# Optimization experiments

Hardware: AMD Instinct MI355X
Metric: run time of the kernel (lower is better)

The kernel has to match this reference:

```python
import jax, jax.numpy as jnp
import numpy as np

B, S, D, H, NK = 2, 512, 256, 8, 16
DK = D // H
NEG = -1e32


def _layer_norm(x, g, b, eps=1e-5):
    m = jnp.mean(x, axis=-1, keepdims=True)
    v = jnp.var(x, axis=-1, keepdims=True)
    return (x - m) / jnp.sqrt(v + eps) * g + b


def _attention(q, k, v, mask, gamma, maxout):
    # q,k,v: [b,h,s,dk]; mask: [1,1,s,s] bool; gamma: [h,1,1]
    d_k = q.shape[-1]
    scores = jnp.einsum('bhqd,bhkd->bhqk', q, k) / float(np.sqrt(d_k))
    s = scores.shape[-1]
    # gamma exp-decay branch (at=None in practice -> position_effect path)
    sm = jax.nn.softmax(jnp.where(mask, scores, NEG), axis=-1)
    distcum = jnp.cumsum(sm, axis=-1)
    disttotal = jnp.sum(sm, axis=-1, keepdims=True)
    idx = jnp.arange(s, dtype=scores.dtype)
    pos = jnp.abs(idx[None, :] - idx[:, None])[None, None]  # |x1 - x2|
    dist = jax.lax.stop_gradient(
        jnp.sqrt(jnp.clip((disttotal - distcum) * pos, 0.0, None)))
    g = -jnp.abs(gamma)[None]  # [1,h,1,1]
    total_effect = jnp.clip(jnp.exp(dist * g), 1e-5, 1e5)
    scores = scores * total_effect
    scores = jax.nn.softmax(jnp.where(mask, scores, NEG), axis=-1)
    scores = jnp.where(mask, scores, 0.0)
    if maxout:
        scale = jnp.minimum(1.0 / jnp.max(scores, axis=-1, keepdims=True), 5.0)
        scores = scores * scale
    out = jnp.einsum('bhqk,bhkd->bhqd', scores, v)
    return out, scores


def _mha(qx, kx, vx, mask, Wq, bq, Wk, bk, Wv, bv, Wo, bo, gammas, maxout):
    b, s, d = qx.shape
    def proj(x, W, bb):
        return (x @ W.T + bb).reshape(b, s, H, DK).transpose(0, 2, 1, 3)
    q = proj(qx, Wq, bq)
    k = proj(kx, Wk, bk)
    v = proj(vx, Wv, bv)
    out, scores = _attention(q, k, v, mask, gammas, maxout)
    concat = out.transpose(0, 2, 1, 3).reshape(b, s, d)
    return concat @ Wo.T + bo, scores


def _layer(qx, kx, vx, mask, Wq, bq, Wk, bk, Wv, bv, Wo, bo, gammas, ln_g, ln_b, maxout):
    out, scores = _mha(qx, kx, vx, mask, Wq, bq, Wk, bk, Wv, bv, Wo, bo, gammas, maxout)
    return _layer_norm(qx + out, ln_g, ln_b), scores  # dropout=identity in eval


def setup_inputs() -> dict:
    key = jax.random.key(0)
    ks = iter(jax.random.split(key, 40))
    def W(shp, sc=0.05):
        return jax.random.normal(next(ks), shp, jnp.float32) * sc
    return dict(
        q_emb=jax.random.normal(next(ks), (B, S, D), jnp.float32),
        s_emb=jax.random.normal(next(ks), (B, S, D), jnp.float32),
        s_emb_extr=jax.random.normal(next(ks), (B, S, D), jnp.float32),
        lens=jax.random.randint(next(ks), (B,), 1, S),
        at=jax.random.randint(next(ks), (B, S), 0, 300),
        Wq1=W((D, D)), bq1=jnp.zeros((D,)), Wv1=W((D, D)), bv1=jnp.zeros((D,)),
        Wo1=W((D, D)), bo1=jnp.zeros((D,)), gam1=W((H, 1, 1), 0.3),
        ln1_g=jnp.ones((D,)), ln1_b=jnp.zeros((D,)),
        Wq4=W((D, D)), bq4=jnp.zeros((D,)), Wk4=W((D, D)), bk4=jnp.zeros((D,)),
        Wv4=W((D, D)), bv4=jnp.zeros((D,)),
        Wo4=W((D, D)), bo4=jnp.zeros((D,)), gam4=W((H, 1, 1), 0.3),
        ln4_g=jnp.ones((D,)), ln4_b=jnp.zeros((D,)),
        know_params=jax.random.uniform(next(ks), (NK, D), jnp.float32, -1.0, 1.0),
    )


def reference(q_emb, s_emb, s_emb_extr, lens, at,
              Wq1, bq1, Wv1, bv1, Wo1, bo1, gam1, ln1_g, ln1_b,
              Wq4, bq4, Wk4, bk4, Wv4, bv4, Wo4, bo4, gam4, ln4_g, ln4_b,
              know_params):
    bs, s, d = q_emb.shape
    tri = jnp.tril(jnp.ones((s, s), bool), 0)[None, None]       # peek_cur=True
    tri_strict = jnp.tril(jnp.ones((s, s), bool), -1)[None, None]  # peek_cur=False
    # block1: kq_same -> k_linear is q_linear; maxout=False
    p, q_scores = _layer(q_emb, q_emb, s_emb, tri,
                         Wq1, bq1, Wq1, bq1, Wv1, bv1, Wo1, bo1, gam1,
                         ln1_g, ln1_b, maxout=False)
    # expand knowledge queries: [bs*NK, s, d]
    query = jnp.broadcast_to(know_params[None, :, None, :], (bs, NK, s, d)).reshape(bs * NK, s, d)
    hq = jnp.broadcast_to(q_emb[:, None], (bs, NK, s, d)).reshape(bs * NK, s, d)
    pe = jnp.broadcast_to(p[:, None], (bs, NK, s, d)).reshape(bs * NK, s, d)
    # block4: kq_same=False; maxout=True
    z, k_scores = _layer(query, hq, pe, tri_strict,
                         Wq4, bq4, Wk4, bk4, Wv4, bv4, Wo4, bo4, gam4,
                         ln4_g, ln4_b, maxout=True)
    z = z.reshape(bs, NK, s, d).transpose(0, 2, 1, 3).reshape(bs, s, NK * d)
    k_scores = k_scores.reshape(bs, NK, H, s, s).transpose(0, 2, 3, 1, 4)
    return z, q_scores, k_scores
```

## Files before the change

### kernel.cpp

```cpp
#include <hip/hip_runtime.h>


namespace {
constexpr int kB = 2, kS = 512, kD = 256, kH = 8, kDK = 32, kNK = 16;
constexpr float kScale = 0.17677669529663687f;
constexpr int kPS = 520;
}

typedef unsigned short u16;
typedef u16 u16x4 __attribute__((ext_vector_type(4)));
typedef u16 u16x8 __attribute__((ext_vector_type(8)));
typedef short s16x8 __attribute__((ext_vector_type(8)));
typedef float f32x4 __attribute__((ext_vector_type(4)));

__device__ __forceinline__ float bf2f(u16 u) { return __uint_as_float(((unsigned)u) << 16); }
__device__ __forceinline__ u16 f2bf(float f) {
    unsigned u = __float_as_uint(f);
    return (u16)((u + 0x7fffu + ((u >> 16) & 1u)) >> 16);
}

__device__ __forceinline__ float wave_max64(float v) {
#pragma unroll
    for (int off = 32; off; off >>= 1) v = fmaxf(v, __shfl_xor(v, off));
    return v;
}
__device__ __forceinline__ float wave_sum64(float v) {
#pragma unroll
    for (int off = 32; off; off >>= 1) v += __shfl_xor(v, off);
    return v;
}

__global__ __launch_bounds__(256) void wt_kernel(const float* __restrict__ W0,
                                                 const float* __restrict__ W1,
                                                 const float* __restrict__ W2,
                                                 const float* __restrict__ W3,
                                                 const float* __restrict__ W4,
                                                 const float* __restrict__ W5,
                                                 float* __restrict__ WT) {
    const float* srcs[6] = {W0, W1, W2, W3, W4, W5};
    const float* W = srcs[blockIdx.y];
    float* T = WT + (size_t)blockIdx.y * kD * kD;
    const int k = blockIdx.x, c = threadIdx.x;
    T[(size_t)k * kD + c] = W[(size_t)c * kD + k];
}

__global__ __launch_bounds__(256) void vt4_kernel(const float* __restrict__ V4,
                                                  u16* __restrict__ Vtg) {
    __shared__ float tile[128][33];
    const int bh = blockIdx.x, kt = blockIdx.y;
    const int t = threadIdx.x;
    const float* src = V4 + ((size_t)bh * kS + kt * 128) * kDK;
    for (int i = t * 4; i < 128 * 32; i += 1024) {
        f32x4 v = *(const f32x4*)(src + i);
        const int k = i >> 5, d = i & 31;
        tile[k][d] = v[0]; tile[k][d + 1] = v[1];
        tile[k][d + 2] = v[2]; tile[k][d + 3] = v[3];
    }
    __syncthreads();
    const int d = t >> 3, kc = (t & 7) * 16;
    u16* dst = Vtg + ((size_t)bh * kDK + d) * kS + kt * 128 + kc;
    u16x8 o1, o2;
#pragma unroll
    for (int j = 0; j < 8; ++j) o1[j] = f2bf(tile[kc + j][d]);
#pragma unroll
    for (int j = 0; j < 8; ++j) o2[j] = f2bf(tile[kc + 8 + j][d]);
    *(u16x8*)dst = o1;
    *(u16x8*)(dst + 8) = o2;
}

template <int RPW, int MODE>
__global__ __launch_bounds__(256) void gemm256(const float* __restrict__ X,
                                               const float* __restrict__ WT,
                                               const float* __restrict__ bias,
                                               const float* __restrict__ extra,
                                               const float* __restrict__ lng,
                                               const float* __restrict__ lnb,
                                               float* __restrict__ Y) {
    constexpr int TM = RPW * 4;
    __shared__ float xs[TM][kD];
    const int t = threadIdx.x;
    const int r0 = blockIdx.x * TM;

    if (MODE == 0) {
#pragma unroll
        for (int it = 0; it < RPW; ++it) {
            const int idx = it * 1024 + t * 4;
            const int r = idx >> 8, c = idx & 255;
            *(f32x4*)&xs[r][c] = *(const f32x4*)(X + (size_t)(r0 + r) * kD + c);
        }
    } else {
#pragma unroll
        for (int it = 0; it < RPW; ++it) {
            const int chunk = it * 32 + (t >> 3);
            const int r = chunk >> 3, h = chunk & 7;
            const int row = r0 + r;
            const float* src = X + (((size_t)(row >> 9) * kH + h) * kS + (row & (kS - 1))) * kDK + (t & 7) * 4;
            *(f32x4*)&xs[r][h * kDK + (t & 7) * 4] = *(const f32x4*)src;
        }
    }
    __syncthreads();

    const int wv = t >> 6;
    const int c4 = (t & 63) * 4;
    float acc[RPW][4];
    {
        f32x4 bv = *(const f32x4*)(bias + c4);
#pragma unroll
        for (int r = 0; r < RPW; ++r)
#pragma unroll
            for (int j = 0; j < 4; ++j) acc[r][j] = bv[j];
    }
    for (int k0 = 0; k0 < kD; k0 += 4) {
        f32x4 w0 = *(const f32x4*)(WT + (size_t)(k0 + 0) * kD + c4);
        f32x4 w1 = *(const f32x4*)(WT + (size_t)(k0 + 1) * kD + c4);
        f32x4 w2 = *(const f32x4*)(WT + (size_t)(k0 + 2) * kD + c4);
        f32x4 w3 = *(const f32x4*)(WT + (size_t)(k0 + 3) * kD + c4);
#pragma unroll
        for (int r = 0; r < RPW; ++r) {
            f32x4 xv = *(const f32x4*)&xs[wv * RPW + r][k0];
#pragma unroll
            for (int cc = 0; cc < 4; ++cc) {
                acc[r][cc] = fmaf(xv[0], w0[cc], acc[r][cc]);
                acc[r][cc] = fmaf(xv[1], w1[cc], acc[r][cc]);
                acc[r][cc] = fmaf(xv[2], w2[cc], acc[r][cc]);
                acc[r][cc] = fmaf(xv[3], w3[cc], acc[r][cc]);
            }
        }
    }

#pragma unroll
    for (int r = 0; r < RPW; ++r) {
        const int row = r0 + wv * RPW + r;
        if (MODE == 0) {
            const int h = c4 >> 5, dk = c4 & 31;
            *(f32x4*)(Y + (((size_t)(row >> 9) * kH + h) * kS + (row & (kS - 1))) * kDK + dk) =
                *(f32x4*)acc[r];
        } else {
            f32x4 x;
            if (MODE == 1) {
                f32x4 e = *(const f32x4*)(extra + (size_t)row * kD + c4);
#pragma unroll
                for (int j = 0; j < 4; ++j) x[j] = acc[r][j] + e[j];
            } else {
                const int nk = (row >> 9) & (kNK - 1);
                f32x4 e = *(const f32x4*)(extra + (size_t)nk * kD + c4);
#pragma unroll
                for (int j = 0; j < 4; ++j) x[j] = acc[r][j] + e[j];
            }
            float s1 = x[0] + x[1] + x[2] + x[3];
            float s2 = x[0] * x[0] + x[1] * x[1] + x[2] * x[2] + x[3] * x[3];
#pragma unroll
            for (int off = 32; off; off >>= 1) {
                s1 += __shfl_xor(s1, off);
                s2 += __shfl_xor(s2, off);
            }
            const float mean = s1 * (1.f / kD);
            const float var = s2 * (1.f / kD) - mean * mean;
            const float rstd = rsqrtf(var + 1e-5f);
            f32x4 g = *(const f32x4*)(lng + c4);
            f32x4 bb = *(const f32x4*)(lnb + c4);
            f32x4 y;
#pragma unroll
            for (int j = 0; j < 4; ++j) y[j] = (x[j] - mean) * rstd * g[j] + bb[j];
            if (MODE == 1) {
                *(f32x4*)(Y + (size_t)row * kD + c4) = y;
            } else {
                const int bnk = row >> 9, s = row & (kS - 1);
                const int nk = bnk & (kNK - 1), b = bnk >> 4;
                *(f32x4*)(Y + (((size_t)(b * kS + s) * kNK + nk) * kD) + c4) = y;
            }
        }
    }
}

__global__ __launch_bounds__(256) void gemm256_b3(const float* __restrict__ X0,
                                                  const float* __restrict__ WT0,
                                                  const float* __restrict__ b0,
                                                  float* __restrict__ Y0,
                                                  const float* __restrict__ X1,
                                                  const float* __restrict__ WT1,
                                                  const float* __restrict__ b1,
                                                  float* __restrict__ Y1,
                                                  const float* __restrict__ X2,
                                                  const float* __restrict__ WT2,
                                                  const float* __restrict__ b2,
                                                  float* __restrict__ Y2) {
    __shared__ float xs[4][kD];
    const float* X = (blockIdx.y == 0) ? X0 : (blockIdx.y == 1) ? X1 : X2;
    const float* WT = (blockIdx.y == 0) ? WT0 : (blockIdx.y == 1) ? WT1 : WT2;
    const float* bias = (blockIdx.y == 0) ? b0 : (blockIdx.y == 1) ? b1 : b2;
    float* Y = (blockIdx.y == 0) ? Y0 : (blockIdx.y == 1) ? Y1 : Y2;
    const int t = threadIdx.x;
    const int r0 = blockIdx.x * 4;

    {
        const int idx = t * 4;
        const int r = idx >> 8, c = idx & 255;
        *(f32x4*)&xs[r][c] = *(const f32x4*)(X + (size_t)(r0 + r) * kD + c);
    }
    __syncthreads();

    const int wv = t >> 6;
    const int c4 = (t & 63) * 4;
    float acc[4];
    {
        f32x4 bv = *(const f32x4*)(bias + c4);
#pragma unroll
        for (int j = 0; j < 4; ++j) acc[j] = bv[j];
    }
    for (int k0 = 0; k0 < kD; k0 += 4) {
        f32x4 w0 = *(const f32x4*)(WT + (size_t)(k0 + 0) * kD + c4);
        f32x4 w1 = *(const f32x4*)(WT + (size_t)(k0 + 1) * kD + c4);
        f32x4 w2 = *(const f32x4*)(WT + (size_t)(k0 + 2) * kD + c4);
        f32x4 w3 = *(const f32x4*)(WT + (size_t)(k0 + 3) * kD + c4);
        f32x4 xv = *(const f32x4*)&xs[wv][k0];
#pragma unroll
        for (int cc = 0; cc < 4; ++cc) {
            acc[cc] = fmaf(xv[0], w0[cc], acc[cc]);
            acc[cc] = fmaf(xv[1], w1[cc], acc[cc]);
            acc[cc] = fmaf(xv[2], w2[cc], acc[cc]);
            acc[cc] = fmaf(xv[3], w3[cc], acc[cc]);
        }
    }
    const int row = r0 + wv;
    const int h = c4 >> 5, dk = c4 & 31;
    *(f32x4*)(Y + (((size_t)(row >> 9) * kH + h) * kS + (row & (kS - 1))) * kDK + dk) =
        *(f32x4*)acc;
}

__global__ __launch_bounds__(256) void proj_kernel(const float* __restrict__ X,
                                                   const float* __restrict__ W,
                                                   const float* __restrict__ bias,
                                                   float* __restrict__ Y, int scatter) {
    const int row = blockIdx.x;
    const int c = threadIdx.x;
    __shared__ float xs[kD];
    xs[c] = X[(size_t)row * kD + c];
    __syncthreads();
    float acc = bias[c];
    const float* wr = W + (size_t)c * kD;
#pragma unroll 4
    for (int k0 = 0; k0 < kD; k0 += 4) {
        f32x4 wv = *(const f32x4*)(wr + k0);
#pragma unroll
        for (int j = 0; j < 4; ++j) acc = fmaf(xs[k0 + j], wv[j], acc);
    }
    if (scatter) {
        const int b = row >> 9, s = row & (kS - 1);
        const int h = c >> 5, dk = c & 31;
        Y[((size_t)(b * kH + h) * kS + s) * kDK + dk] = acc;
    } else {
        Y[(size_t)row * kD + c] = acc;
    }
}

__global__ __launch_bounds__(256) void attn1_kernel(const float* __restrict__ Q1,
                                                    const float* __restrict__ V1,
                                                    const float* __restrict__ gam,
                                                    float* __restrict__ q_scores,
                                                    float* __restrict__ A1) {
    extern __shared__ char smem[];
    float* Sl = (float*)smem;
    u16* Vt = (u16*)(smem + 32 * 536 * 4);
    u16* Pl = (u16*)(smem + 32 * 536 * 4 + 32 * kPS * 2);

    const int bh = blockIdx.x;
    const int q0 = blockIdx.y * 32;
    const int h = bh & (kH - 1);
    const int tid = threadIdx.x;
    const int lane = tid & 63;
    const int w = tid >> 6;
    const float* Kb = Q1 + (size_t)bh * kS * kDK;
    const float* Vb = V1 + (size_t)bh * kS * kDK;

#pragma unroll
    for (int it = 0; it < 16; ++it) {
        const int idx = it * 1024 + tid * 4;
        const int k = idx >> 5, d = idx & 31;
        f32x4 v = *(const f32x4*)(Vb + idx);
        Vt[(d + 0) * kPS + k] = f2bf(v[0]);
        Vt[(d + 1) * kPS + k] = f2bf(v[1]);
        Vt[(d + 2) * kPS + k] = f2bf(v[2]);
        Vt[(d + 3) * kPS + k] = f2bf(v[3]);
    }

    {
        const int qt = w & 1, khalf = w >> 1;
        const int qrow = q0 + qt * 16 + (lane & 15);
        const int dof = (lane >> 4) * 8;
        f32x4 qa = *(const f32x4*)(Kb + (size_t)qrow * kDK + dof);
        f32x4 qb = *(const f32x4*)(Kb + (size_t)qrow * kDK + dof + 4);
        s16x8 aq_h, aq_l;
#pragma unroll
        for (int j = 0; j < 4; ++j) {
            float f = qa[j];
            u16 hi = f2bf(f);
            aq_h[j] = (short)hi;
            aq_l[j] = (short)f2bf(f - bf2f(hi));
            f = qb[j];
            hi = f2bf(f);
            aq_h[4 + j] = (short)hi;
            aq_l[4 + j] = (short)f2bf(f - bf2f(hi));
        }
        for (int kt = khalf * 16; kt < khalf * 16 + 16; ++kt) {
            const int krow = kt * 16 + (lane & 15);
            f32x4 ka = *(const f32x4*)(Kb + (size_t)krow * kDK + dof);
            f32x4 kb2 = *(const f32x4*)(Kb + (size_t)krow * kDK + dof + 4);
            s16x8 bk_h, bk_l;
#pragma unroll
            for (int j = 0; j < 4; ++j) {
                float f = ka[j];
                u16 hi = f2bf(f);
                bk_h[j] = (short)hi;
                bk_l[j] = (short)f2bf(f - bf2f(hi));
                f = kb2[j];
                hi = f2bf(f);
                bk_h[4 + j] = (short)hi;
                bk_l[4 + j] = (short)f2bf(f - bf2f(hi));
            }
            f32x4 acc = {0.f, 0.f, 0.f, 0.f};
            acc = __builtin_amdgcn_mfma_f32_16x16x32_bf16(aq_h, bk_h, acc, 0, 0, 0);
            acc = __builtin_amdgcn_mfma_f32_16x16x32_bf16(aq_l, bk_h, acc, 0, 0, 0);
            acc = __builtin_amdgcn_mfma_f32_16x16x32_bf16(aq_h, bk_l, acc, 0, 0, 0);
            const int colk = kt * 16 + (lane & 15);
            const int seg = colk >> 6, ii = colk & 63;
#pragma unroll
            for (int j = 0; j < 4; ++j) {
                const int row = qt * 16 + (lane >> 4) * 4 + j;
                Sl[row * 536 + seg * 67 + ii] = acc[j] * kScale;
            }
        }
    }
    __syncthreads();

    const float gh = -fabsf(gam[h]);
    {
        const int r = tid >> 3, seg = tid & 7;
        const int q = q0 + r, L = q + 1, ks = seg * 64;
        const float* srow = Sl + r * 536 + seg * 67;
        float sv[64];
#pragma unroll
        for (int i = 0; i < 64; ++i) sv[i] = srow[i];
        const int nv = min(max(L - ks, 0), 64);
        float m = -3e38f;
#pragma unroll
        for (int i = 0; i < 64; ++i)
            if (i < nv) m = fmaxf(m, sv[i]);
#pragma unroll
        for (int off = 1; off < 8; off <<= 1) m = fmaxf(m, __shfl_xor(m, off));
        float segsum = 0.f;
#pragma unroll
        for (int i = 0; i < 64; ++i)
            if (i < nv) segsum += __expf(sv[i] - m);
        float tot = segsum;
#pragma unroll
        for (int off = 1; off < 8; off <<= 1) tot += __shfl_xor(tot, off);
        float inc = segsum;
#pragma unroll
        for (int off = 1; off < 8; off <<= 1) {
            const float tmp = __shfl_up(inc, off);
            if ((tid & 7) >= off) inc += tmp;
        }
        float run = inc - segsum;
        const float inv_tot = 1.f / tot;
        float m2 = -3e38f;
#pragma unroll
        for (int i = 0; i < 64; ++i) {
            if (i < nv) {
                const float E = __expf(sv[i] - m);
                run += E;
                const float rem = 1.f - run * inv_tot;
                const float pos = (float)(q - (ks + i));
                const float val = fmaxf(rem * pos, 0.f);
                const float te = fmaxf(__expf(gh * sqrtf(val)), 1e-5f);
                const float s2 = sv[i] * te;
                sv[i] = s2;
                m2 = fmaxf(m2, s2);
            }
        }
#pragma unroll
        for (int off = 1; off < 8; off <<= 1) m2 = fmaxf(m2, __shfl_xor(m2, off));
        float sum2 = 0.f;
#pragma unroll
        for (int i = 0; i < 64; ++i) {
            const float p = (i < nv) ? __expf(sv[i] - m2) : 0.f;
            sv[i] = p;
            sum2 += p;
        }
#pragma unroll
        for (int off = 1; off < 8; off <<= 1) sum2 += __shfl_xor(sum2, off);
        const float inv2 = 1.f / sum2;
        float* qrow = q_scores + ((size_t)bh * kS + q) * kS + ks;
        u16* prow = Pl + r * kPS + ks;
#pragma unroll
        for (int i = 0; i < 64; i += 4) {
            f32x4 o;
            u16x4 pb;
#pragma unroll
            for (int j = 0; j < 4; ++j) {
                const float p = sv[i + j] * inv2;
                o[j] = p;
                pb[j] = f2bf(p);
            }
            *(f32x4*)(qrow + i) = o;
            *(u16x4*)(prow + i) = pb;
        }
    }
    __syncthreads();

    {
        const int qt = w & 1, dt = w >> 1;
        const u16* Arow = Pl + (size_t)(qt * 16 + (lane & 15)) * kPS + (lane >> 4) * 8;
        const u16* Brow = Vt + (size_t)(dt * 16 + (lane & 15)) * kPS + (lane >> 4) * 8;
        f32x4 acc = {0.f, 0.f, 0.f, 0.f};
#pragma unroll
        for (int kc = 0; kc < kS; kc += 32) {
            s16x8 a = *(const s16x8*)(Arow + kc);
            s16x8 b = *(const s16x8*)(Brow + kc);
            acc = __builtin_amdgcn_mfma_f32_16x16x32_bf16(a, b, acc, 0, 0, 0);
        }
        const int d = dt * 16 + (lane & 15);
#pragma unroll
        for (int j = 0; j < 4; ++j) {
            const int row = qt * 16 + (lane >> 4) * 4 + j;
            A1[((size_t)bh * kS + (q0 + row)) * kDK + d] = acc[j];
        }
    }
}

__global__ __launch_bounds__(64) void attn4_prep(const float* __restrict__ Q4,
                                                 const float* __restrict__ K4,
                                                 float* __restrict__ rawP,
                                                 float* __restrict__ CpreP) {
    const int panel = blockIdx.x;
    const int h = panel & (kH - 1);
    const int bnk = panel >> 3;
    const int nk = bnk & (kNK - 1);
    const int b = bnk >> 4;
    const int lane = threadIdx.x;
    const float* Kp = K4 + (size_t)(b * kH + h) * kS * kDK;
    float qv[kDK];
    const float* Qr = Q4 + (size_t)nk * kD + h * kDK;
#pragma unroll
    for (int d = 0; d < kDK; ++d) qv[d] = Qr[d];

    const int k0 = lane * 8;
    float raw[8];
    float m = -3e38f;
#pragma unroll
    for (int j = 0; j < 8; ++j) {
        const float* kr = Kp + (size_t)(k0 + j) * kDK;
        float s = 0.f;
#pragma unroll
        for (int d = 0; d < kDK; ++d) s = fmaf(qv[d], kr[d], s);
        raw[j] = s * kScale;
        m = fmaxf(m, raw[j]);
    }
    m = wave_max64(m);
    float E[8];
    float s = 0.f;
#pragma unroll
    for (int j = 0; j < 8; ++j) { E[j] = __expf(raw[j] - m); s += E[j]; }
    float inc = s;
#pragma unroll
    for (int off = 1; off < 64; off <<= 1) {
        float t = __shfl_up(inc, off);
        if (lane >= off) inc += t;
    }
    float run = inc - s;
    float cp[8];
#pragma unroll
    for (int j = 0; j < 8; ++j) { run += E[j]; cp[j] = run; }

    float* rrow = rawP + (size_t)panel * kS + k0;
    float* crow = CpreP + (size_t)panel * kS + k0;
    *(f32x4*)(rrow) = *(f32x4*)(raw);
    *(f32x4*)(rrow + 4) = *(f32x4*)(raw + 4);
    *(f32x4*)(crow) = *(f32x4*)(cp);
    *(f32x4*)(crow + 4) = *(f32x4*)(cp + 4);
}

__global__ __launch_bounds__(256) void attn4_main(const float* __restrict__ rawP,
                                                  const float* __restrict__ CpreP,
                                                  const u16* __restrict__ Vtg,
                                                  const float* __restrict__ gam,
                                                  float* __restrict__ k_scores,
                                                  float* __restrict__ A4) {
    extern __shared__ char smem[];
    u16* Pl = (u16*)smem;
    float* raws_l = (float*)(smem + 32 * kPS * 2);
    float* cps_l = raws_l + kS;

    const int panel = blockIdx.x;
    const int q0 = blockIdx.y * 32;
    const int h = panel & (kH - 1);
    const int bnk = panel >> 3;
    const int nk = bnk & (kNK - 1);
    const int b = bnk >> 4;
    const int tid = threadIdx.x;
    const int lane = tid & 63;
    const int w = tid >> 6;

    for (int i = tid; i < kS; i += 256) {
        raws_l[i] = rawP[(size_t)panel * kS + i];
        cps_l[i] = CpreP[(size_t)panel * kS + i];
    }
    __syncthreads();

    const float gh = -fabsf(gam[h]);
    const int rbase = w * 8;
    const int k0 = lane * 8;
    float rw[8], cp[8];
    *(f32x4*)(rw) = *(const f32x4*)(raws_l + k0);
    *(f32x4*)(rw + 4) = *(const f32x4*)(raws_l + k0 + 4);
    *(f32x4*)(cp) = *(const f32x4*)(cps_l + k0);
    *(f32x4*)(cp + 4) = *(const f32x4*)(cps_l + k0 + 4);

    for (int r = 0; r < 8; ++r) {
        const int row = rbase + r;
        const int Lr = q0 + row;
        float* krow = k_scores + ((size_t)((b * kH + h) * kS + Lr) * kNK + nk) * kS;
        u16* prow = Pl + (size_t)row * kPS + k0;
        if (Lr == 0) {
            f32x4 z = {0.f, 0.f, 0.f, 0.f};
            *(f32x4*)(krow + k0) = z;
            *(f32x4*)(krow + k0 + 4) = z;
            u16x8 zb = {0, 0, 0, 0, 0, 0, 0, 0};
            *(u16x8*)(prow) = zb;
            continue;
        }
        const float invCL = 1.f / cps_l[Lr - 1];
        const float fL = (float)(Lr - k0);
        float s2v[8];
        float mloc = -3e38f;
#pragma unroll
        for (int j = 0; j < 8; ++j) {
            const float rem = 1.f - cp[j] * invCL;
            const float val = fmaxf(rem * (fL - (float)j), 0.f);
            const float te = fmaxf(__expf(gh * sqrtf(val)), 1e-5f);
            const float s2 = rw[j] * te;
            s2v[j] = s2;
            if (k0 + j < Lr) mloc = fmaxf(mloc, s2);
        }
        const float m2 = wave_max64(mloc);
        float p[8];
        float psum = 0.f;
#pragma unroll
        for (int j = 0; j < 8; ++j) {
            p[j] = (k0 + j < Lr) ? __expf(s2v[j] - m2) : 0.f;
            psum += p[j];
        }
        const float sum2 = wave_sum64(psum);
        const float scl = fminf(sum2, 5.f) / sum2;
        u16x8 pb;
#pragma unroll
        for (int j = 0; j < 8; ++j) {
            p[j] *= scl;
            pb[j] = f2bf(p[j]);
        }
        *(f32x4*)(krow + k0) = *(f32x4*)(p);
        *(f32x4*)(krow + k0 + 4) = *(f32x4*)(p + 4);
        *(u16x8*)(prow) = pb;
    }
    __syncthreads();

    const int rowblk = (w & 1) * 16;
    const int dblk = (w >> 1) * 16;
    const u16* Arow = Pl + (size_t)(rowblk + (lane & 15)) * kPS + (lane >> 4) * 8;
    const u16* Brow = Vtg + ((size_t)(b * kH + h) * kDK + dblk + (lane & 15)) * kS + (lane >> 4) * 8;
    f32x4 acc = {0.f, 0.f, 0.f, 0.f};
#pragma unroll
    for (int kc = 0; kc < kS; kc += 32) {
        s16x8 a = *(const s16x8*)(Arow + kc);
        s16x8 bfr = *(const s16x8*)(Brow + kc);
        acc = __builtin_amdgcn_mfma_f32_16x16x32_bf16(a, bfr, acc, 0, 0, 0);
    }
    const int d = dblk + (lane & 15);
#pragma unroll
    for (int j = 0; j < 4; ++j) {
        const int row = rowblk + (lane >> 4) * 4 + j;
        A4[((size_t)panel * kS + (q0 + row)) * kDK + d] = acc[j];
    }
}

extern "C" void kernel_launch(void* const* d_in, const int* in_sizes, int n_in,
                              void* d_out, int out_size, void* d_ws, size_t ws_size,
                              hipStream_t stream) {
    (void)in_sizes; (void)n_in; (void)out_size; (void)ws_size;

    const float* q_emb = (const float*)d_in[0];
    const float* s_emb = (const float*)d_in[1];
    const float* Wq1 = (const float*)d_in[5];  const float* bq1 = (const float*)d_in[6];
    const float* Wv1 = (const float*)d_in[7];  const float* bv1 = (const float*)d_in[8];
    const float* Wo1 = (const float*)d_in[9];  const float* bo1 = (const float*)d_in[10];
    const float* gam1 = (const float*)d_in[11];
    const float* ln1g = (const float*)d_in[12]; const float* ln1b = (const float*)d_in[13];
    const float* Wq4 = (const float*)d_in[14]; const float* bq4 = (const float*)d_in[15];
    const float* Wk4 = (const float*)d_in[16]; const float* bk4 = (const float*)d_in[17];
    const float* Wv4 = (const float*)d_in[18]; const float* bv4 = (const float*)d_in[19];
    const float* Wo4 = (const float*)d_in[20]; const float* bo4 = (const float*)d_in[21];
    const float* gam4 = (const float*)d_in[22];
    const float* ln4g = (const float*)d_in[23]; const float* ln4b = (const float*)d_in[24];
    const float* know = (const float*)d_in[25];

    float* ws = (float*)d_ws;
    const size_t NBHSD = (size_t)kB * kH * kS * kDK;
    float* Q1 = ws;
    float* V1 = Q1 + NBHSD;
    float* A1 = V1 + NBHSD;
    float* P  = A1 + NBHSD;
    float* K4 = P  + (size_t)kB * kS * kD;
    float* V4 = K4 + NBHSD;
    float* Q4 = V4 + NBHSD;
    float* A4 = Q4 + (size_t)kNK * kD;
    float* WT = A4 + (size_t)kB * kNK * kH * kS * kDK;
    u16* Vtg = (u16*)(WT + 6 * (size_t)kD * kD);

    float* rawP = V1;
    float* CpreP = V1 + (size_t)kB * kNK * kH * kS;

    float* WTq1 = WT + 0 * (size_t)kD * kD;
    float* WTv1 = WT + 1 * (size_t)kD * kD;
    float* WTo1 = WT + 2 * (size_t)kD * kD;
    float* WTk4 = WT + 3 * (size_t)kD * kD;
    float* WTv4 = WT + 4 * (size_t)kD * kD;
    float* WTo4 = WT + 5 * (size_t)kD * kD;

    float* zout = (float*)d_out;
    float* q_scores = zout + (size_t)kB * kS * kNK * kD;
    float* k_scores = q_scores + (size_t)kB * kH * kS * kS;

    {
        dim3 g(kD, 6);
        wt_kernel<<<g, 256, 0, stream>>>(Wq1, Wv1, Wo1, Wk4, Wv4, Wo4, WT);
    }
    {
        dim3 g(kB * kS / 4, 3);
        gemm256_b3<<<g, 256, 0, stream>>>(q_emb, WTq1, bq1, Q1,
                                          s_emb, WTv1, bv1, V1,
                                          q_emb, WTk4, bk4, K4);
    }
    proj_kernel<<<kNK, 256, 0, stream>>>(know, Wq4, bq4, Q4, 0);

    {
        dim3 g1(kB * kH, kS / 32);
        const int lds1 = 32 * 536 * 4 + 2 * 32 * kPS * 2;
        attn1_kernel<<<g1, 256, lds1, stream>>>(Q1, V1, gam1, q_scores, A1);
    }
    gemm256<1, 1><<<kB * kS / 4, 256, 0, stream>>>(A1, WTo1, bo1, q_emb, ln1g, ln1b, P);

    gemm256<1, 0><<<kB * kS / 4, 256, 0, stream>>>(P, WTv4, bv4, nullptr, nullptr, nullptr, V4);
    {
        dim3 gv(kB * kH, 4);
        vt4_kernel<<<gv, 256, 0, stream>>>(V4, Vtg);
    }
    attn4_prep<<<kB * kNK * kH, 64, 0, stream>>>(Q4, K4, rawP, CpreP);
    {
        dim3 g5(kB * kNK * kH, kS / 32);
        const int lds_bytes = 32 * kPS * 2 + 2 * kS * 4;
        attn4_main<<<g5, 256, lds_bytes, stream>>>(rawP, CpreP, Vtg, gam4, k_scores, A4);
    }
    gemm256<4, 2><<<kB * kNK * kS / 16, 256, 0, stream>>>(A4, WTo4, bo4, know, ln4g, ln4b, zout);
}
```

Before: 230.2 us.

## Pretranspose V1 globally, shrink attn1 query tile to 16, tile weight transpose

attn1 no longer transposes and converts V into shared memory in every block. A separate vt4_kernel pass writes a bf16 transposed V1 to global memory, and the PV MFMA reads it directly. The query tile per block shrinks from 32 to 16, which cuts LDS use and raises the block count, and the softmax is regrouped as 16 threads per row with 32 columns each. The P buffer reuses the score LDS region after an extra barrier. The weight transpose kernel now uses a 32x32 shared tile for coalesced access, and attn4_prep loads K with vectorized float4 reads. The trade-off is one extra kernel launch, and only two of the four waves do the PV product.

```diff
diff --git a/kernel.cpp b/kernel.cpp
--- a/kernel.cpp
+++ b/kernel.cpp
@@ -5,6 +5,7 @@
 constexpr int kB = 2, kS = 512, kD = 256, kH = 8, kDK = 32, kNK = 16;
 constexpr float kScale = 0.17677669529663687f;
 constexpr int kPS = 520;
+constexpr int kSL = 528;
 }
 
 typedef unsigned short u16;
@@ -37,11 +38,24 @@
                                                  const float* __restrict__ W4,
                                                  const float* __restrict__ W5,
                                                  float* __restrict__ WT) {
+    __shared__ float tile[32][33];
     const float* srcs[6] = {W0, W1, W2, W3, W4, W5};
     const float* W = srcs[blockIdx.y];
     float* T = WT + (size_t)blockIdx.y * kD * kD;
-    const int k = blockIdx.x, c = threadIdx.x;
-    T[(size_t)k * kD + c] = W[(size_t)c * kD + k];
+    const int tx = blockIdx.x & 7, ty = blockIdx.x >> 3;
+    const int t = threadIdx.x;
+    {
+        const int cl = t >> 3, kl = (t & 7) * 4;
+        f32x4 v = *(const f32x4*)(W + (size_t)(ty * 32 + cl) * kD + tx * 32 + kl);
+        tile[cl][kl] = v[0]; tile[cl][kl + 1] = v[1];
+        tile[cl][kl + 2] = v[2]; tile[cl][kl + 3] = v[3];
+    }
+    __syncthreads();
+    {
+        const int kl = t >> 3, cl = (t & 7) * 4;
+        f32x4 o = {tile[cl][kl], tile[cl + 1][kl], tile[cl + 2][kl], tile[cl + 3][kl]};
+        *(f32x4*)(T + (size_t)(tx * 32 + kl) * kD + ty * 32 + cl) = o;
+    }
 }
 
 __global__ __launch_bounds__(256) void vt4_kernel(const float* __restrict__ V4,
@@ -255,38 +269,24 @@
 }
 
 __global__ __launch_bounds__(256) void attn1_kernel(const float* __restrict__ Q1,
-                                                    const float* __restrict__ V1,
+                                                    const u16* __restrict__ Vtg1,
                                                     const float* __restrict__ gam,
                                                     float* __restrict__ q_scores,
                                                     float* __restrict__ A1) {
     extern __shared__ char smem[];
     float* Sl = (float*)smem;
-    u16* Vt = (u16*)(smem + 32 * 536 * 4);
-    u16* Pl = (u16*)(smem + 32 * 536 * 4 + 32 * kPS * 2);
+    u16* Pl = (u16*)smem;
 
     const int bh = blockIdx.x;
-    const int q0 = blockIdx.y * 32;
+    const int q0 = blockIdx.y * 16;
     const int h = bh & (kH - 1);
     const int tid = threadIdx.x;
     const int lane = tid & 63;
     const int w = tid >> 6;
     const float* Kb = Q1 + (size_t)bh * kS * kDK;
-    const float* Vb = V1 + (size_t)bh * kS * kDK;
-
-#pragma unroll
-    for (int it = 0; it < 16; ++it) {
-        const int idx = it * 1024 + tid * 4;
-        const int k = idx >> 5, d = idx & 31;
-        f32x4 v = *(const f32x4*)(Vb + idx);
-        Vt[(d + 0) * kPS + k] = f2bf(v[0]);
-        Vt[(d + 1) * kPS + k] = f2bf(v[1]);
-        Vt[(d + 2) * kPS + k] = f2bf(v[2]);
-        Vt[(d + 3) * kPS + k] = f2bf(v[3]);
-    }
-
-    {
-        const int qt = w & 1, khalf = w >> 1;
-        const int qrow = q0 + qt * 16 + (lane & 15);
+
+    {
+        const int qrow = q0 + (lane & 15);
         const int dof = (lane >> 4) * 8;
         f32x4 qa = *(const f32x4*)(Kb + (size_t)qrow * kDK + dof);
         f32x4 qb = *(const f32x4*)(Kb + (size_t)qrow * kDK + dof + 4);
@@ -302,7 +302,7 @@
             aq_h[4 + j] = (short)hi;
             aq_l[4 + j] = (short)f2bf(f - bf2f(hi));
         }
-        for (int kt = khalf * 16; kt < khalf * 16 + 16; ++kt) {
+        for (int kt = w * 8; kt < w * 8 + 8; ++kt) {
             const int krow = kt * 16 + (lane & 15);
             f32x4 ka = *(const f32x4*)(Kb + (size_t)krow * kDK + dof);
             f32x4 kb2 = *(const f32x4*)(Kb + (size_t)krow * kDK + dof + 4);
@@ -323,49 +323,52 @@
             acc = __builtin_amdgcn_mfma_f32_16x16x32_bf16(aq_l, bk_h, acc, 0, 0, 0);
             acc = __builtin_amdgcn_mfma_f32_16x16x32_bf16(aq_h, bk_l, acc, 0, 0, 0);
             const int colk = kt * 16 + (lane & 15);
-            const int seg = colk >> 6, ii = colk & 63;
+            const int seg = colk >> 5, ii = colk & 31;
 #pragma unroll
             for (int j = 0; j < 4; ++j) {
-                const int row = qt * 16 + (lane >> 4) * 4 + j;
-                Sl[row * 536 + seg * 67 + ii] = acc[j] * kScale;
+                const int row = (lane >> 4) * 4 + j;
+                Sl[row * kSL + seg * 33 + ii] = acc[j] * kScale;
             }
         }
     }
     __syncthreads();
 
     const float gh = -fabsf(gam[h]);
-    {
-        const int r = tid >> 3, seg = tid & 7;
-        const int q = q0 + r, L = q + 1, ks = seg * 64;
-        const float* srow = Sl + r * 536 + seg * 67;
-        float sv[64];
-#pragma unroll
-        for (int i = 0; i < 64; ++i) sv[i] = srow[i];
-        const int nv = min(max(L - ks, 0), 64);
+    const int r = tid >> 4, seg16 = tid & 15;
+    const int q = q0 + r, L = q + 1, ks = seg16 * 32;
+    float sv[32];
+    {
+        const float* srow = Sl + r * kSL + seg16 * 33;
+#pragma unroll
+        for (int i = 0; i < 32; ++i) sv[i] = srow[i];
+    }
+    __syncthreads();
+    {
+        const int nv = min(max(L - ks, 0), 32);
         float m = -3e38f;
 #pragma unroll
-        for (int i = 0; i < 64; ++i)
+        for (int i = 0; i < 32; ++i)
             if (i < nv) m = fmaxf(m, sv[i]);
 #pragma unroll
-        for (int off = 1; off < 8; off <<= 1) m = fmaxf(m, __shfl_xor(m, off));
+        for (int off = 1; off < 16; off <<= 1) m = fmaxf(m, __shfl_xor(m, off));
         float segsum = 0.f;
 #pragma unroll
-        for (int i = 0; i < 64; ++i)
+        for (int i = 0; i < 32; ++i)
             if (i < nv) segsum += __expf(sv[i] - m);
         float tot = segsum;
 #pragma unroll
-        for (int off = 1; off < 8; off <<= 1) tot += __shfl_xor(tot, off);
+        for (int off = 1; off < 16; off <<= 1) tot += __shfl_xor(tot, off);
         float inc = segsum;
 #pragma unroll
-        for (int off = 1; off < 8; off <<= 1) {
+        for (int off = 1; off < 16; off <<= 1) {
             const float tmp = __shfl_up(inc, off);
-            if ((tid & 7) >= off) inc += tmp;
+            if ((tid & 15) >= off) inc += tmp;
         }
         float run = inc - segsum;
         const float inv_tot = 1.f / tot;
         float m2 = -3e38f;
 #pragma unroll
-        for (int i = 0; i < 64; ++i) {
+        for (int i = 0; i < 32; ++i) {
             if (i < nv) {
                 const float E = __expf(sv[i] - m);
                 run += E;
@@ -379,21 +382,21 @@
             }
         }
 #pragma unroll
-        for (int off = 1; off < 8; off <<= 1) m2 = fmaxf(m2, __shfl_xor(m2, off));
+        for (int off = 1; off < 16; off <<= 1) m2 = fmaxf(m2, __shfl_xor(m2, off));
         float sum2 = 0.f;
 #pragma unroll
-        for (int i = 0; i < 64; ++i) {
+        for (int i = 0; i < 32; ++i) {
             const float p = (i < nv) ? __expf(sv[i] - m2) : 0.f;
             sv[i] = p;
             sum2 += p;
         }
 #pragma unroll
-        for (int off = 1; off < 8; off <<= 1) sum2 += __shfl_xor(sum2, off);
+        for (int off = 1; off < 16; off <<= 1) sum2 += __shfl_xor(sum2, off);
         const float inv2 = 1.f / sum2;
         float* qrow = q_scores + ((size_t)bh * kS + q) * kS + ks;
         u16* prow = Pl + r * kPS + ks;
 #pragma unroll
-        for (int i = 0; i < 64; i += 4) {
+        for (int i = 0; i < 32; i += 4) {
             f32x4 o;
             u16x4 pb;
 #pragma unroll
@@ -408,10 +411,10 @@
     }
     __syncthreads();
 
-    {
-        const int qt = w & 1, dt = w >> 1;
-        const u16* Arow = Pl + (size_t)(qt * 16 + (lane & 15)) * kPS + (lane >> 4) * 8;
-        const u16* Brow = Vt + (size_t)(dt * 16 + (lane & 15)) * kPS + (lane >> 4) * 8;
+    if (w < 2) {
+        const int dt = w;
+        const u16* Arow = Pl + (size_t)(lane & 15) * kPS + (lane >> 4) * 8;
+        const u16* Brow = Vtg1 + ((size_t)bh * kDK + dt * 16 + (lane & 15)) * kS + (lane >> 4) * 8;
         f32x4 acc = {0.f, 0.f, 0.f, 0.f};
 #pragma unroll
         for (int kc = 0; kc < kS; kc += 32) {
@@ -422,7 +425,7 @@
         const int d = dt * 16 + (lane & 15);
 #pragma unroll
         for (int j = 0; j < 4; ++j) {
-            const int row = qt * 16 + (lane >> 4) * 4 + j;
+            const int row = (lane >> 4) * 4 + j;
             A1[((size_t)bh * kS + (q0 + row)) * kDK + d] = acc[j];
         }
     }
@@ -452,7 +455,13 @@
         const float* kr = Kp + (size_t)(k0 + j) * kDK;
         float s = 0.f;
 #pragma unroll
-        for (int d = 0; d < kDK; ++d) s = fmaf(qv[d], kr[d], s);
+        for (int d4 = 0; d4 < 8; ++d4) {
+            f32x4 kv = *(const f32x4*)(kr + d4 * 4);
+            s = fmaf(qv[d4 * 4 + 0], kv[0], s);
+            s = fmaf(qv[d4 * 4 + 1], kv[1], s);
+            s = fmaf(qv[d4 * 4 + 2], kv[2], s);
+            s = fmaf(qv[d4 * 4 + 3], kv[3], s);
+        }
         raw[j] = s * kScale;
         m = fmaxf(m, raw[j]);
     }
@@ -615,6 +624,7 @@
     float* A4 = Q4 + (size_t)kNK * kD;
     float* WT = A4 + (size_t)kB * kNK * kH * kS * kDK;
     u16* Vtg = (u16*)(WT + 6 * (size_t)kD * kD);
+    u16* Vtg1 = Vtg + (size_t)kB * kH * kDK * kS;
 
     float* rawP = V1;
     float* CpreP = V1 + (size_t)kB * kNK * kH * kS;
@@ -631,7 +641,7 @@
     float* k_scores = q_scores + (size_t)kB * kH * kS * kS;
 
     {
-        dim3 g(kD, 6);
+        dim3 g(64, 6);
         wt_kernel<<<g, 256, 0, stream>>>(Wq1, Wv1, Wo1, Wk4, Wv4, Wo4, WT);
     }
     {
@@ -641,11 +651,15 @@
                                           q_emb, WTk4, bk4, K4);
     }
     proj_kernel<<<kNK, 256, 0, stream>>>(know, Wq4, bq4, Q4, 0);
-
-    {
-        dim3 g1(kB * kH, kS / 32);
-        const int lds1 = 32 * 536 * 4 + 2 * 32 * kPS * 2;
-        attn1_kernel<<<g1, 256, lds1, stream>>>(Q1, V1, gam1, q_scores, A1);
+    {
+        dim3 gv(kB * kH, 4);
+        vt4_kernel<<<gv, 256, 0, stream>>>(V1, Vtg1);
+    }
+
+    {
+        dim3 g1(kB * kH, kS / 16);
+        const int lds1 = 16 * kSL * 4;
+        attn1_kernel<<<g1, 256, lds1, stream>>>(Q1, Vtg1, gam1, q_scores, A1);
     }
     gemm256<1, 1><<<kB * kS / 4, 256, 0, stream>>>(A1, WTo1, bo1, q_emb, ln1g, ln1b, P);
 
```

New measurement: 230.7 us. About the same (+0.2%).
